# Kernel optimization log

Hardware: AMD Instinct MI355X
Metric: run time of the kernel (lower is better)

The kernel has to match this reference:

```python
import jax, jax.numpy as jnp
import numpy as np

# ---- config (matches init_kwargs: seek_thermal, K=1024 points, P=5 persons) ----
H, W = 150, 200
N = H * W
K = 1024          # max_num_points
P = 5             # max_num_persons
HFOV_DEG, VFOV_DEG = 81.0, 59.0
DEPTH_MIN = 3.0   # valid depth threshold
BIG = 1e9         # sentinel for invalid depths when sorting


def _camera_rays():
    fx = W / (2.0 * np.tan(np.deg2rad(HFOV_DEG) / 2.0))
    fy = H / (2.0 * np.tan(np.deg2rad(VFOV_DEG) / 2.0))
    x, y = np.meshgrid(np.arange(W, dtype=np.float32), np.arange(H, dtype=np.float32), indexing='xy')
    x_cam = (x - W / 2.0) / fx   # (H, W)
    y_cam = (y - H / 2.0) / fy   # (H, W)
    return jnp.asarray(x_cam), jnp.asarray(y_cam)


def _masked_quantile(d_sorted, n, q):
    # linear-interpolation quantile over the first n sorted entries (torch.quantile default)
    pos = q * jnp.maximum(n.astype(d_sorted.dtype) - 1.0, 0.0)          # (B, P)
    lo = jnp.floor(pos).astype(jnp.int32)
    hi = jnp.ceil(pos).astype(jnp.int32)
    frac = pos - lo.astype(d_sorted.dtype)
    vlo = jnp.take_along_axis(d_sorted, lo[..., None], axis=-1)[..., 0]
    vhi = jnp.take_along_axis(d_sorted, hi[..., None], axis=-1)[..., 0]
    return vlo + (vhi - vlo) * frac


def setup_inputs() -> dict:
    key = jax.random.key(0)
    k1, k2, k3 = jax.random.split(key, 3)
    B = 128
    depth = jax.random.uniform(k1, (B, H, W), dtype=jnp.float32) * 8.0            # depths 0..8m
    indicator = jax.random.randint(k2, (B, H, W), 0, P + 1).astype(jnp.float32)   # person ids 0..P
    extra = jax.random.normal(k3, (B, H, W), dtype=jnp.float32)                   # unused channel
    depth_mask_3C = jnp.stack([depth, indicator, extra], axis=1)                  # (B, 3, H, W)
    return {"depth_mask_3C": depth_mask_3C}


def reference(depth_mask_3C) -> jnp.ndarray:
    B = depth_mask_3C.shape[0]
    dtype = depth_mask_3C.dtype
    x_cam, y_cam = _camera_rays()

    depth = depth_mask_3C[:, 0].reshape(B, N)                         # (B, N)
    indicator = jnp.round(depth_mask_3C[:, 1]).reshape(B, N)          # (B, N)

    # per-person membership masks, persons 1..P
    pids = jnp.arange(1, P + 1, dtype=dtype)
    mask = indicator[:, None, :] == pids[None, :, None]               # (B, P, N)
    valid = mask & (depth[:, None, :] > DEPTH_MIN)                    # (B, P, N)

    # grouped IQR outlier bounds via masked sort + interpolated quantile
    d = jnp.where(valid, depth[:, None, :], BIG)
    d_sorted = jnp.sort(d, axis=-1)                                   # (B, P, N)
    n_valid = valid.sum(axis=-1)                                      # (B, P)
    q1 = _masked_quantile(d_sorted, n_valid, 0.25)
    q3 = _masked_quantile(d_sorted, n_valid, 0.75)
    iqr = q3 - q1
    lb = (q1 - 1.5 * iqr)[..., None]
    ub = (q3 + 1.5 * iqr)[..., None]
    keep = valid & (depth[:, None, :] >= lb) & (depth[:, None, :] <= ub)   # (B, P, N)

    # 3D points: (x_cam*z, y_cam*z, z) per pixel
    rays = jnp.stack([x_cam.reshape(N), y_cam.reshape(N), jnp.ones((N,), dtype)], axis=-1)  # (N, 3)
    pts = depth[..., None] * rays[None]                               # (B, N, 3)

    # deterministic variant of sampling: take the first K kept points in raster order
    rank = jnp.cumsum(keep.astype(jnp.int32), axis=-1) - 1            # (B, P, N)
    idx = jnp.where(keep & (rank < K), rank, K)                       # overflow/invalid -> slot K (discarded)

    def fill(idx_p, pts_b):                                           # idx_p (N,), pts_b (N, 3)
        return jnp.zeros((K + 1, 3), dtype).at[idx_p].set(pts_b)[:K]

    buf = jax.vmap(lambda i_b, p_b: jax.vmap(fill, in_axes=(0, None))(i_b, p_b))(idx, pts)  # (B, P, K, 3)

    # presence flag goes into slot K, channel 0
    flag = (keep.sum(axis=-1) > 0).astype(dtype)                      # (B, P)
    extra = flag[..., None, None] * jnp.array([1.0, 0.0, 0.0], dtype) # (B, P, 1, 3)
    seg = jnp.concatenate([buf, extra], axis=2)                       # (B, P, K+1, 3)
    return jnp.transpose(seg, (0, 3, 1, 2)).reshape(B, 3, P * (K + 1))
```

## Files before the change

kernel.cpp:

```cpp
#include <hip/hip_runtime.h>
#include <math.h>

#define HGT 150
#define WID 200
#define NPIX 30000
#define NF4  7500
#define KMAX 1024
#define PMAX 5
#define THREADS 512
#define NWAVES 8
#define CAPW 512
#define CAP  (NWAVES*CAPW)
#define NWORDS 938
#define NWPAD 940
#define NBIN 2048
#define SHIFT 13
#define KBASE 0x40400000u
#define GCAP 128
#define STRIDE_C (PMAX*(KMAX+1))

__device__ __forceinline__ uint32_t wave_incl_scan(uint32_t x, int lane) {
#pragma unroll
    for (int off = 1; off < 64; off <<= 1) {
        uint32_t y = __shfl_up(x, (unsigned)off, 64);
        if (lane >= off) x += y;
    }
    return x;
}
__device__ __forceinline__ uint32_t wave_red_add(uint32_t x) {
#pragma unroll
    for (int off = 32; off >= 1; off >>= 1) x += __shfl_xor(x, off, 64);
    return x;
}
__device__ __forceinline__ uint32_t key_bin(uint32_t key) {
    uint32_t d = (key - KBASE) >> SHIFT;
    return d < NBIN ? d : (NBIN - 1);
}

__device__ void locate_ranks(const uint32_t* hh, int seg, const uint32_t* s_rank,
                             uint32_t* s_tbin, uint32_t* s_tbel, uint32_t* s_ws) {
    const int tid = threadIdx.x, lane = tid & 63, wv = tid >> 6;
    const uint32_t* mine = hh + tid * seg;
    uint32_t segsum = 0;
    for (int j = 0; j < seg; ++j) segsum += mine[j];
    uint32_t inc = wave_incl_scan(segsum, lane);
    if (lane == 63) s_ws[wv] = inc;
    __syncthreads();
    uint32_t tbase = inc - segsum;
    for (int w = 0; w < wv; ++w) tbase += s_ws[w];
#pragma unroll
    for (int k = 0; k < 4; ++k) {
        uint32_t r = s_rank[k];
        if (r >= tbase && r < tbase + segsum) {
            uint32_t c = tbase;
            for (int j = 0; j < seg; ++j) {
                uint32_t h = mine[j];
                if (r < c + h) { s_tbin[k] = (uint32_t)(tid * seg + j); s_tbel[k] = c; break; }
                c += h;
            }
        }
    }
    __syncthreads();
}

__global__ __launch_bounds__(THREADS, 4) void fused(const float* __restrict__ in,
                                                    float* __restrict__ out, int B) {
    const int nbp = B * PMAX;
    int x = blockIdx.x, b, p;
    if ((nbp & 7) == 0) {
        int per = nbp >> 3;
        int slot = (x & 7) * per + (x >> 3);
        b = slot / PMAX; p = slot - b * PMAX;
    } else { b = x / PMAX; p = x - b * PMAX; }

    const float pid = (float)(p + 1);
    const float4* __restrict__ depth4 = (const float4*)(in + (size_t)b * 3 * NPIX);
    const float4* __restrict__ ind4   = depth4 + NF4;
    const int tid = threadIdx.x, lane = tid & 63, wv = tid >> 6;

    __shared__ uint2 list[CAP];
    __shared__ uint32_t hist[NBIN];
    __shared__ uint32_t vb2[NWPAD];
    __shared__ unsigned short wpfx[NWPAD];
    __shared__ float xc_tab[WID];
    __shared__ float yc_tab[HGT];
    __shared__ uint32_t gbuf[4 * GCAP];
    __shared__ uint32_t gcnt[4];
    __shared__ uint32_t s_ws[NWAVES];
    __shared__ uint32_t s_wcnt[NWAVES];
    __shared__ uint32_t s_rank[4], s_res[4], s_tbin[4], s_tbel[4], s_u[4], s_val[4];
    __shared__ int s_slot[4], s_desc[4];
    __shared__ uint32_t s_dprefix, s_dr;

    for (int i = tid; i < NBIN; i += THREADS) hist[i] = 0;
    for (int i = tid; i < NWPAD; i += THREADS) vb2[i] = 0;
    {
        const double fxd = (double)WID / (2.0 * tan((81.0 * M_PI / 180.0) * 0.5));
        const double fyd = (double)HGT / (2.0 * tan((59.0 * M_PI / 180.0) * 0.5));
        for (int i = tid; i < WID; i += THREADS) xc_tab[i] = (float)(((double)i - (double)WID / 2.0) / fxd);
        for (int i = tid; i < HGT; i += THREADS) yc_tab[i] = (float)(((double)i - (double)HGT / 2.0) / fyd);
    }
    __syncthreads();

    const uint32_t segbase = (uint32_t)wv * CAPW;
    const uint32_t seglim = segbase + CAPW;
    uint32_t run = 0;
#pragma unroll 5
    for (int k = 0; k < 15; ++k) {
        int f = k * THREADS + tid;
        uint32_t nib = 0;
        float4 d4;
        if (f < NF4) {
            d4 = depth4[f];
            float4 i4 = ind4[f];
            const float* dd = (const float*)&d4;
            const float* ii = (const float*)&i4;
#pragma unroll
            for (int j = 0; j < 4; ++j)
                if (rintf(ii[j]) == pid && dd[j] > 3.0f) nib |= 1u << j;
        }
        uint32_t cnt_t = (uint32_t)__popc(nib);
        uint32_t incl = wave_incl_scan(cnt_t, lane);
        uint32_t wtot = __shfl(incl, 63, 64);
        uint32_t pos = segbase + run + incl - cnt_t;
        run += wtot;
        if (nib) {
            const float* dd = (const float*)&d4;
#pragma unroll
            for (int j = 0; j < 4; ++j)
                if ((nib >> j) & 1u) {
                    uint32_t key = __float_as_uint(dd[j]);
                    atomicAdd(&hist[key_bin(key)], 1u);
                    if (pos < seglim) list[pos] = make_uint2(key, (uint32_t)(f * 4 + j));
                    ++pos;
                }
        }
    }
    if (lane == 0) s_wcnt[wv] = run;
    __syncthreads();

    uint32_t n = 0;
    bool over = false;
#pragma unroll
    for (int w = 0; w < NWAVES; ++w) {
        uint32_t c = s_wcnt[w];
        n += c;
        over |= (c > CAPW);
    }

    float* outB = out + (size_t)b * 3 * STRIDE_C + p * (KMAX + 1);

    if (n == 0) {
        for (int r = tid; r <= KMAX; r += THREADS) {
            outB[r] = 0.f; outB[STRIDE_C + r] = 0.f; outB[2 * STRIDE_C + r] = 0.f;
        }
        return;
    }

    uint32_t rank[4]; float posf[2];
    {
        float nf = (float)n;
        posf[0] = 0.25f * fmaxf(nf - 1.0f, 0.0f);
        posf[1] = 0.75f * fmaxf(nf - 1.0f, 0.0f);
        rank[0] = (uint32_t)floorf(posf[0]); rank[1] = (uint32_t)ceilf(posf[0]);
        rank[2] = (uint32_t)floorf(posf[1]); rank[3] = (uint32_t)ceilf(posf[1]);
    }

    if (over) {
        uint32_t v[4];
        for (int k = 0; k < 4; ++k) {
            if (tid == 0) { s_dprefix = 0; s_dr = rank[k]; }
            __syncthreads();
            for (int bit = 30; bit >= 0; --bit) {
                uint32_t pfx = s_dprefix;
                uint32_t c = 0;
                for (int kk = 0; kk < 15; ++kk) {
                    int f = kk * THREADS + tid;
                    if (f < NF4) {
                        float4 d4 = depth4[f]; float4 i4 = ind4[f];
                        const float* dd = (const float*)&d4;
                        const float* ii = (const float*)&i4;
#pragma unroll
                        for (int j = 0; j < 4; ++j)
                            if (rintf(ii[j]) == pid && dd[j] > 3.0f) {
                                uint32_t key = __float_as_uint(dd[j]);
                                if ((key >> (bit + 1)) == pfx && !((key >> bit) & 1u)) ++c;
                            }
                    }
                }
                c = wave_red_add(c);
                if (lane == 0) s_ws[wv] = c;
                __syncthreads();
                uint32_t c0 = 0;
                for (int w = 0; w < NWAVES; ++w) c0 += s_ws[w];
                if (tid == 0) {
                    if (s_dr < c0) s_dprefix = pfx << 1;
                    else { s_dprefix = (pfx << 1) | 1u; s_dr -= c0; }
                }
                __syncthreads();
            }
            v[k] = s_dprefix;
            __syncthreads();
        }
        float f1 = posf[0] - floorf(posf[0]);
        float f3 = posf[1] - floorf(posf[1]);
        float q1 = __uint_as_float(v[0]) + (__uint_as_float(v[1]) - __uint_as_float(v[0])) * f1;
        float q3 = __uint_as_float(v[2]) + (__uint_as_float(v[3]) - __uint_as_float(v[2])) * f3;
        float iqr = q3 - q1;
        float lb = q1 - 1.5f * iqr, ub = q3 + 1.5f * iqr;
        if (tid == 0) {
            const float* depth = (const float*)depth4;
            const float* ind = (const float*)ind4;
            uint32_t r = 0;
            for (int i = 0; i < NPIX; ++i) {
                float d = depth[i];
                if (rintf(ind[i]) == pid && d > 3.0f && d >= lb && d <= ub) {
                    if (r < KMAX) {
                        int row = i / WID, col = i - row * WID;
                        outB[r] = xc_tab[col] * d;
                        outB[STRIDE_C + r] = yc_tab[row] * d;
                        outB[2 * STRIDE_C + r] = d;
                    }
                    ++r;
                }
            }
            s_dr = r;
        }
        __syncthreads();
        uint32_t count = s_dr;
        uint32_t start = count < KMAX ? count : KMAX;
        for (uint32_t r = start + tid; r < KMAX; r += THREADS) {
            outB[r] = 0.f; outB[STRIDE_C + r] = 0.f; outB[2 * STRIDE_C + r] = 0.f;
        }
        if (tid == 0) {
            outB[KMAX] = (count > 0) ? 1.0f : 0.0f;
            outB[STRIDE_C + KMAX] = 0.f; outB[2 * STRIDE_C + KMAX] = 0.f;
        }
        return;
    }

    const uint32_t wn = s_wcnt[wv];

    if (tid == 0) {
#pragma unroll
        for (int k = 0; k < 4; ++k) s_rank[k] = rank[k];
    }
    __syncthreads();
    locate_ranks(hist, NBIN / THREADS, s_rank, s_tbin, s_tbel, s_ws);

    if (tid == 0) {
        uint32_t uq[4]; int nu = 0;
#pragma unroll
        for (int k = 0; k < 4; ++k) {
            s_res[k] = rank[k] - s_tbel[k];
            int fnd = -1;
            for (int u = 0; u < nu; ++u) if (uq[u] == s_tbin[k]) fnd = u;
            if (fnd < 0) { uq[nu] = s_tbin[k]; fnd = nu; ++nu; }
            s_slot[k] = fnd;
        }
#pragma unroll
        for (int u = 0; u < 4; ++u) { s_u[u] = 0xFFFFFFFFu; gcnt[u] = 0; }
        for (int u = 0; u < nu; ++u) if (hist[uq[u]] <= GCAP) s_u[u] = uq[u];
#pragma unroll
        for (int k = 0; k < 4; ++k) s_desc[k] = (hist[uq[s_slot[k]]] > GCAP) ? 1 : 0;
    }
    __syncthreads();

    for (uint32_t i = segbase + lane; i < segbase + wn; i += 64) {
        uint32_t key = list[i].x;
        uint32_t bin = key_bin(key);
#pragma unroll
        for (int u = 0; u < 4; ++u)
            if (bin == s_u[u]) {
                uint32_t slot = atomicAdd(&gcnt[u], 1u);
                if (slot < GCAP) gbuf[u * GCAP + slot] = key;
            }
    }
    __syncthreads();
    if (wv < 4 && !s_desc[wv]) {
        int u = s_slot[wv];
        uint32_t c = gcnt[u];
        uint32_t res = s_res[wv];
        for (uint32_t i = lane; i < c; i += 64) {
            uint32_t xk = gbuf[u * GCAP + i];
            uint32_t less = 0, eq = 0;
            for (uint32_t j = 0; j < c; ++j) {
                uint32_t y = gbuf[u * GCAP + j];
                less += (y < xk); eq += (y == xk);
            }
            if (res >= less && res < less + eq) s_val[wv] = xk;
        }
    }
    __syncthreads();
    for (int k = 0; k < 4; ++k) if (s_desc[k]) {
        if (tid == 0) { s_dprefix = 0; s_dr = rank[k]; }
        __syncthreads();
        for (int bit = 30; bit >= 0; --bit) {
            uint32_t pfx = s_dprefix;
            uint32_t c = 0;
            for (uint32_t i = segbase + lane; i < segbase + wn; i += 64) {
                uint32_t key = list[i].x;
                if ((key >> (bit + 1)) == pfx && !((key >> bit) & 1u)) ++c;
            }
            c = wave_red_add(c);
            if (lane == 0) s_ws[wv] = c;
            __syncthreads();
            uint32_t c0 = 0;
            for (int w = 0; w < NWAVES; ++w) c0 += s_ws[w];
            if (tid == 0) {
                if (s_dr < c0) s_dprefix = pfx << 1;
                else { s_dprefix = (pfx << 1) | 1u; s_dr -= c0; }
            }
            __syncthreads();
        }
        if (tid == 0) s_val[k] = s_dprefix;
        __syncthreads();
    }

    float lb, ub;
    {
        float f1 = posf[0] - floorf(posf[0]);
        float f3 = posf[1] - floorf(posf[1]);
        float v0 = __uint_as_float(s_val[0]), v1 = __uint_as_float(s_val[1]);
        float v2 = __uint_as_float(s_val[2]), v3 = __uint_as_float(s_val[3]);
        float q1 = v0 + (v1 - v0) * f1;
        float q3 = v2 + (v3 - v2) * f3;
        float iqr = q3 - q1;
        lb = q1 - 1.5f * iqr;
        ub = q3 + 1.5f * iqr;
    }

    for (uint32_t i = segbase + lane; i < segbase + wn; i += 64) {
        uint2 e = list[i];
        float d = __uint_as_float(e.x);
        if (d >= lb && d <= ub) atomicOr(&vb2[e.y >> 5], 1u << (e.y & 31));
    }
    __syncthreads();
    {
        uint4 v4 = make_uint4(0, 0, 0, 0);
        if (tid < NWPAD / 4) v4 = ((const uint4*)vb2)[tid];
        uint32_t pc0 = (uint32_t)__popc(v4.x), pc1 = (uint32_t)__popc(v4.y);
        uint32_t pc2 = (uint32_t)__popc(v4.z), pc3 = (uint32_t)__popc(v4.w);
        uint32_t lsum = pc0 + pc1 + pc2 + pc3;
        uint32_t inc = wave_incl_scan(lsum, lane);
        if (lane == 63) s_ws[wv] = inc;
        __syncthreads();
        uint32_t rn = inc - lsum;
        for (int w = 0; w < wv; ++w) rn += s_ws[w];
        if (tid < NWPAD / 4) {
            ushort4 w4;
            w4.x = (unsigned short)rn;            rn += pc0;
            w4.y = (unsigned short)rn;            rn += pc1;
            w4.z = (unsigned short)rn;            rn += pc2;
            w4.w = (unsigned short)rn;
            ((ushort4*)wpfx)[tid] = w4;
        }
    }
    __syncthreads();
    uint32_t total = 0;
    for (int w = 0; w < NWAVES; ++w) total += s_ws[w];

    for (uint32_t i = segbase + lane; i < segbase + wn; i += 64) {
        uint2 e = list[i];
        float d = __uint_as_float(e.x);
        if (d >= lb && d <= ub) {
            uint32_t s = e.y;
            uint32_t w = s >> 5;
            uint32_t r = (uint32_t)wpfx[w] + (uint32_t)__popc(vb2[w] & ((1u << (s & 31)) - 1u));
            if (r < KMAX) {
                uint32_t row = s / WID;
                uint32_t col = s - row * WID;
                outB[r] = xc_tab[col] * d;
                outB[STRIDE_C + r] = yc_tab[row] * d;
                outB[2 * STRIDE_C + r] = d;
            }
        }
    }
    uint32_t start = total < KMAX ? total : KMAX;
    for (uint32_t r = start + tid; r < KMAX; r += THREADS) {
        outB[r] = 0.f; outB[STRIDE_C + r] = 0.f; outB[2 * STRIDE_C + r] = 0.f;
    }
    if (tid == 0) {
        outB[KMAX] = (total > 0) ? 1.0f : 0.0f;
        outB[STRIDE_C + KMAX] = 0.f;
        outB[2 * STRIDE_C + KMAX] = 0.f;
    }
}

extern "C" void kernel_launch(void* const* d_in, const int* in_sizes, int n_in,
                              void* d_out, int out_size, void* d_ws, size_t ws_size,
                              hipStream_t stream) {
    (void)n_in; (void)out_size; (void)d_ws; (void)ws_size;
    const float* in = (const float*)d_in[0];
    float* out = (float*)d_out;
    const int B = in_sizes[0] / (3 * NPIX);
    fused<<<B * PMAX, THREADS, 0, stream>>>(in, out, B);
}
```

Measured before the change: 100.0 us.

## Shrink shared-memory footprint and batch loads three at a time in the compaction loop

Splits the uint2 candidate list into a 32-bit key array and a 16-bit pixel-index array, and halves the histogram bin count by widening the shift. Both cut LDS usage, which may allow more resident blocks. The scan loop now processes three float4 loads per wave scan, so there are fewer scans and more loads in flight. The vb2 bitmap clear moves into waves that are otherwise idle during the rank-select step, and output writes skip the popcount when the word prefix already exceeds K. Coarser bins can leave more candidates in a target bin, pushing more cases onto the slower bit-by-bit fallback, and the extra registers may limit occupancy.

```diff
diff --git a/kernel.cpp b/kernel.cpp
--- a/kernel.cpp
+++ b/kernel.cpp
@@ -13,8 +13,8 @@
 #define CAP  (NWAVES*CAPW)
 #define NWORDS 938
 #define NWPAD 940
-#define NBIN 2048
-#define SHIFT 13
+#define NBIN 1024
+#define SHIFT 14
 #define KBASE 0x40400000u
 #define GCAP 128
 #define STRIDE_C (PMAX*(KMAX+1))
@@ -78,7 +78,8 @@
     const float4* __restrict__ ind4   = depth4 + NF4;
     const int tid = threadIdx.x, lane = tid & 63, wv = tid >> 6;
 
-    __shared__ uint2 list[CAP];
+    __shared__ uint32_t keys[CAP];
+    __shared__ unsigned short sidx[CAP];
     __shared__ uint32_t hist[NBIN];
     __shared__ uint32_t vb2[NWPAD];
     __shared__ unsigned short wpfx[NWPAD];
@@ -93,7 +94,6 @@
     __shared__ uint32_t s_dprefix, s_dr;
 
     for (int i = tid; i < NBIN; i += THREADS) hist[i] = 0;
-    for (int i = tid; i < NWPAD; i += THREADS) vb2[i] = 0;
     {
         const double fxd = (double)WID / (2.0 * tan((81.0 * M_PI / 180.0) * 0.5));
         const double fyd = (double)HGT / (2.0 * tan((59.0 * M_PI / 180.0) * 0.5));
@@ -105,35 +105,47 @@
     const uint32_t segbase = (uint32_t)wv * CAPW;
     const uint32_t seglim = segbase + CAPW;
     uint32_t run = 0;
-#pragma unroll 5
-    for (int k = 0; k < 15; ++k) {
-        int f = k * THREADS + tid;
-        uint32_t nib = 0;
-        float4 d4;
-        if (f < NF4) {
-            d4 = depth4[f];
-            float4 i4 = ind4[f];
-            const float* dd = (const float*)&d4;
-            const float* ii = (const float*)&i4;
-#pragma unroll
-            for (int j = 0; j < 4; ++j)
-                if (rintf(ii[j]) == pid && dd[j] > 3.0f) nib |= 1u << j;
-        }
-        uint32_t cnt_t = (uint32_t)__popc(nib);
+#pragma unroll
+    for (int g = 0; g < 5; ++g) {
+        float4 dv[3];
+        uint32_t nib[3];
+        uint32_t cnt_t = 0;
+#pragma unroll
+        for (int t = 0; t < 3; ++t) {
+            int f = (g * 3 + t) * THREADS + tid;
+            nib[t] = 0;
+            if (f < NF4) {
+                dv[t] = depth4[f];
+                float4 i4 = ind4[f];
+                const float* dd = (const float*)&dv[t];
+                const float* ii = (const float*)&i4;
+#pragma unroll
+                for (int j = 0; j < 4; ++j)
+                    if (rintf(ii[j]) == pid && dd[j] > 3.0f) nib[t] |= 1u << j;
+                cnt_t += (uint32_t)__popc(nib[t]);
+            }
+        }
         uint32_t incl = wave_incl_scan(cnt_t, lane);
         uint32_t wtot = __shfl(incl, 63, 64);
         uint32_t pos = segbase + run + incl - cnt_t;
         run += wtot;
-        if (nib) {
-            const float* dd = (const float*)&d4;
-#pragma unroll
-            for (int j = 0; j < 4; ++j)
-                if ((nib >> j) & 1u) {
-                    uint32_t key = __float_as_uint(dd[j]);
-                    atomicAdd(&hist[key_bin(key)], 1u);
-                    if (pos < seglim) list[pos] = make_uint2(key, (uint32_t)(f * 4 + j));
-                    ++pos;
-                }
+#pragma unroll
+        for (int t = 0; t < 3; ++t) {
+            if (nib[t]) {
+                int f = (g * 3 + t) * THREADS + tid;
+                const float* dd = (const float*)&dv[t];
+#pragma unroll
+                for (int j = 0; j < 4; ++j)
+                    if ((nib[t] >> j) & 1u) {
+                        uint32_t key = __float_as_uint(dd[j]);
+                        atomicAdd(&hist[key_bin(key)], 1u);
+                        if (pos < seglim) {
+                            keys[pos] = key;
+                            sidx[pos] = (unsigned short)(f * 4 + j);
+                        }
+                        ++pos;
+                    }
+            }
         }
     }
     if (lane == 0) s_wcnt[wv] = run;
@@ -267,7 +279,7 @@
     __syncthreads();
 
     for (uint32_t i = segbase + lane; i < segbase + wn; i += 64) {
-        uint32_t key = list[i].x;
+        uint32_t key = keys[i];
         uint32_t bin = key_bin(key);
 #pragma unroll
         for (int u = 0; u < 4; ++u)
@@ -277,19 +289,23 @@
             }
     }
     __syncthreads();
-    if (wv < 4 && !s_desc[wv]) {
-        int u = s_slot[wv];
-        uint32_t c = gcnt[u];
-        uint32_t res = s_res[wv];
-        for (uint32_t i = lane; i < c; i += 64) {
-            uint32_t xk = gbuf[u * GCAP + i];
-            uint32_t less = 0, eq = 0;
-            for (uint32_t j = 0; j < c; ++j) {
-                uint32_t y = gbuf[u * GCAP + j];
-                less += (y < xk); eq += (y == xk);
-            }
-            if (res >= less && res < less + eq) s_val[wv] = xk;
-        }
+    if (wv < 4) {
+        if (!s_desc[wv]) {
+            int u = s_slot[wv];
+            uint32_t c = gcnt[u];
+            uint32_t res = s_res[wv];
+            for (uint32_t i = lane; i < c; i += 64) {
+                uint32_t xk = gbuf[u * GCAP + i];
+                uint32_t less = 0, eq = 0;
+                for (uint32_t j = 0; j < c; ++j) {
+                    uint32_t y = gbuf[u * GCAP + j];
+                    less += (y < xk); eq += (y == xk);
+                }
+                if (res >= less && res < less + eq) s_val[wv] = xk;
+            }
+        }
+    } else {
+        for (int i = (wv - 4) * 64 + lane; i < NWPAD; i += 256) vb2[i] = 0;
     }
     __syncthreads();
     for (int k = 0; k < 4; ++k) if (s_desc[k]) {
@@ -299,7 +315,7 @@
             uint32_t pfx = s_dprefix;
             uint32_t c = 0;
             for (uint32_t i = segbase + lane; i < segbase + wn; i += 64) {
-                uint32_t key = list[i].x;
+                uint32_t key = keys[i];
                 if ((key >> (bit + 1)) == pfx && !((key >> bit) & 1u)) ++c;
             }
             c = wave_red_add(c);
@@ -331,9 +347,11 @@
     }
 
     for (uint32_t i = segbase + lane; i < segbase + wn; i += 64) {
-        uint2 e = list[i];
-        float d = __uint_as_float(e.x);
-        if (d >= lb && d <= ub) atomicOr(&vb2[e.y >> 5], 1u << (e.y & 31));
+        float d = __uint_as_float(keys[i]);
+        if (d >= lb && d <= ub) {
+            uint32_t s = sidx[i];
+            atomicOr(&vb2[s >> 5], 1u << (s & 31));
+        }
     }
     __syncthreads();
     {
@@ -361,18 +379,21 @@
     for (int w = 0; w < NWAVES; ++w) total += s_ws[w];
 
     for (uint32_t i = segbase + lane; i < segbase + wn; i += 64) {
-        uint2 e = list[i];
-        float d = __uint_as_float(e.x);
+        uint32_t key = keys[i];
+        float d = __uint_as_float(key);
         if (d >= lb && d <= ub) {
-            uint32_t s = e.y;
+            uint32_t s = sidx[i];
             uint32_t w = s >> 5;
-            uint32_t r = (uint32_t)wpfx[w] + (uint32_t)__popc(vb2[w] & ((1u << (s & 31)) - 1u));
-            if (r < KMAX) {
-                uint32_t row = s / WID;
-                uint32_t col = s - row * WID;
-                outB[r] = xc_tab[col] * d;
-                outB[STRIDE_C + r] = yc_tab[row] * d;
-                outB[2 * STRIDE_C + r] = d;
+            uint32_t base = wpfx[w];
+            if (base < KMAX) {
+                uint32_t r = base + (uint32_t)__popc(vb2[w] & ((1u << (s & 31)) - 1u));
+                if (r < KMAX) {
+                    uint32_t row = s / WID;
+                    uint32_t col = s - row * WID;
+                    outB[r] = xc_tab[col] * d;
+                    outB[STRIDE_C + r] = yc_tab[row] * d;
+                    outB[2 * STRIDE_C + r] = d;
+                }
             }
         }
     }
```

After: 98.79 us. No clear change (-1.2%).
